# Optimization experiments

Hardware: AMD Instinct MI355X
Metric: run time of the kernel (lower is better)

The kernel has to match this reference:

```python
import jax, jax.numpy as jnp
import numpy as np
from math import sqrt

B, L, S, H, E, D = 2, 2048, 2048, 16, 64, 64

def setup_inputs() -> dict:
    key = jax.random.key(0)
    kq, kk, kv = jax.random.split(key, 3)
    queries = jax.random.normal(kq, (B, L, H, E), dtype=jnp.float32)
    keys = jax.random.normal(kk, (B, S, H, E), dtype=jnp.float32)
    values = jax.random.normal(kv, (B, S, H, D), dtype=jnp.float32)
    # causal mask: True where attention is NOT allowed (j > i), matching masked_fill_ semantics
    causal = jnp.triu(jnp.ones((L, S), dtype=jnp.bool_), k=1)
    attn_mask = jnp.broadcast_to(causal[None, None, :, :], (B, 1, L, S))
    return {"queries": queries, "keys": keys, "values": values, "attn_mask": attn_mask}

def reference(queries, keys, values, attn_mask):
    # scores: [B,H,L,S]
    scale = 1.0 / sqrt(queries.shape[-1])
    scores = jnp.einsum('blhe,bshe->bhls', queries, keys)
    scores = jnp.where(attn_mask, -jnp.inf, scores)
    A = jax.nn.softmax(scale * scores, axis=-1)
    V = jnp.einsum('bhls,bshd->blhd', A, values)
    return V
```

## Files before the change

kernel.cpp:

```cpp
#include <hip/hip_runtime.h>

typedef unsigned short ushort_t;
typedef __attribute__((ext_vector_type(8))) short s8v;
typedef __attribute__((ext_vector_type(2))) unsigned u2v;
typedef __attribute__((ext_vector_type(4))) float f4;

__device__ __forceinline__ ushort_t f2bf(float x) {
    unsigned u = __builtin_bit_cast(unsigned, x);
    return (ushort_t)((u + 0x7FFFu + ((u >> 16) & 1u)) >> 16);
}
__device__ __forceinline__ unsigned pack_hi16(float lo, float hi) {
    unsigned a = __builtin_bit_cast(unsigned, lo);
    unsigned b = __builtin_bit_cast(unsigned, hi);
    return (a >> 16) | (b & 0xFFFF0000u);
}

__global__ __launch_bounds__(256) void prep_kv(const float* __restrict__ K,
                                               const float* __restrict__ V,
                                               ushort_t* __restrict__ Kb,
                                               ushort_t* __restrict__ VT) {
    __shared__ ushort_t T[64 * 72];
    if (blockIdx.x < 2048) {
        const int gid = blockIdx.x * 256 + threadIdx.x;
        const int e = (gid & 7) * 8;
        const int h = (gid >> 3) & 15;
        const int s = (gid >> 7) & 2047;
        const int b = gid >> 18;
        const float* src = K + (((b * 2048 + s) * 16 + h) * 64 + e);
        f4 a = *(const f4*)src;
        f4 c = *(const f4*)(src + 4);
        s8v o;
        #pragma unroll
        for (int j = 0; j < 4; ++j) { o[j] = (short)f2bf(a[j]); o[j + 4] = (short)f2bf(c[j]); }
        *(s8v*)(Kb + (((b * 16 + h) * 2048 + s) * 64 + e)) = o;
    } else {
        const int v = blockIdx.x - 2048;
        const int s0 = (v & 31) * 64;
        const int h  = (v >> 5) & 15;
        const int b  = v >> 9;
        const int t  = threadIdx.x;
        {
            const int srow = t >> 2, dc = (t & 3) * 16;
            const float* src = V + (((b * 2048 + s0 + srow) * 16 + h) * 64 + dc);
            #pragma unroll
            for (int c = 0; c < 4; ++c) {
                f4 vv = *(const f4*)(src + c * 4);
                #pragma unroll
                for (int j = 0; j < 4; ++j) T[(dc + c * 4 + j) * 72 + srow] = f2bf(vv[j]);
            }
        }
        __syncthreads();
        {
            const int d = t >> 2, sq = (t & 3) * 16;
            ushort_t* dst = VT + (((b * 16 + h) * 64 + d) * 2048 + s0 + sq);
            *(s8v*)(dst)     = *(const s8v*)(&T[d * 72 + sq]);
            *(s8v*)(dst + 8) = *(const s8v*)(&T[d * 72 + sq + 8]);
        }
    }
}

__global__ __launch_bounds__(128, 2) void fattn_main(
    const float* __restrict__ Q,
    const ushort_t* __restrict__ Kb,
    const ushort_t* __restrict__ VTb,
    float* __restrict__ O)
{
    constexpr float K1 = 0.18033688011112042f;
    constexpr float SHIFT = 12.0f;
    __shared__ ushort_t KT [64 * 72];
    __shared__ ushort_t VTl[64 * 72];
    __shared__ ushort_t P  [4][16 * 72];

    const int bx = blockIdx.x;
    const int bh = bx & 31;
    const int p  = bx >> 5;
    const int b = bh >> 4, h = bh & 15;

    const int wave = threadIdx.x >> 6;
    const int lane = threadIdx.x & 63;
    const int l15  = lane & 15;
    const int quad = lane >> 4;

    const ushort_t* kb  = Kb  + bh * (2048 * 64);
    const ushort_t* vtb = VTb + bh * (64 * 2048);
    const float*    qb  = Q + b * (2048 * 1024) + h * 64;
    float*          ob  = O + b * (2048 * 1024) + h * 64;

    const s8v ones = {0x3F80, 0x3F80, 0x3F80, 0x3F80, 0x3F80, 0x3F80, 0x3F80, 0x3F80};
    const f4 zero4 = {0.f, 0.f, 0.f, 0.f};

    const int sr = (wave << 5) + (lane >> 1);
    const int sc = (lane & 1) << 5;

    int qr0 = p * 64;

    s8v aq[2][2];
    f4 oacc[2][4];
    f4 lsum[2];

    auto loadQ = [&](int qr) {
        #pragma unroll
        for (int m = 0; m < 2; ++m) {
            const float* qrow = qb + (qr + wave * 32 + m * 16 + l15) * 1024;
            #pragma unroll
            for (int ks = 0; ks < 2; ++ks) {
                f4 x = *(const f4*)(qrow + ks * 32 + quad * 8);
                f4 y = *(const f4*)(qrow + ks * 32 + quad * 8 + 4);
                #pragma unroll
                for (int j = 0; j < 4; ++j) {
                    aq[m][ks][j]     = (short)f2bf(x[j]);
                    aq[m][ks][j + 4] = (short)f2bf(y[j]);
                }
            }
        }
    };
    auto zeroAcc = [&]() {
        #pragma unroll
        for (int m = 0; m < 2; ++m) {
            lsum[m] = zero4;
            #pragma unroll
            for (int d = 0; d < 4; ++d) oacc[m][d] = zero4;
        }
    };
    auto storeO = [&](int qr) {
        #pragma unroll
        for (int m = 0; m < 2; ++m)
            #pragma unroll
            for (int r = 0; r < 4; ++r) {
                const float inv = 1.0f / lsum[m][r];
                const int row = qr + wave * 32 + m * 16 + quad * 4 + r;
                #pragma unroll
                for (int dd = 0; dd < 4; ++dd)
                    ob[row * 1024 + dd * 16 + l15] = oacc[m][dd][r] * inv;
            }
    };

    loadQ(qr0);
    zeroAcc();

    s8v gK[4], gV[4];
    {
        const ushort_t* ksrc = kb + sr * 64 + sc;
        const ushort_t* vsrc = vtb + sr * 2048 + sc;
        #pragma unroll
        for (int c = 0; c < 4; ++c) {
            gK[c] = *(const s8v*)(ksrc + c * 8);
            gV[c] = *(const s8v*)(vsrc + c * 8);
        }
    }

    for (int n = 0; n < 33; ++n) {
        #pragma unroll
        for (int c = 0; c < 4; ++c) {
            *(s8v*)&KT [sr * 72 + sc + c * 8] = gK[c];
            *(s8v*)&VTl[sr * 72 + sc + c * 8] = gV[c];
        }
        __syncthreads();

        s8v gK2[4], gV2[4];
        if (n < 32) {
            const int sn = (n + 1 <= p) ? (n + 1) : (n - p);
            const ushort_t* ksrc = kb + (sn * 64 + sr) * 64 + sc;
            const ushort_t* vsrc = vtb + sr * 2048 + sn * 64 + sc;
            #pragma unroll
            for (int c = 0; c < 4; ++c) {
                gK2[c] = *(const s8v*)(ksrc + c * 8);
                gV2[c] = *(const s8v*)(vsrc + c * 8);
            }
        }

        const int s_cur = (n <= p) ? n : (n - p - 1);
        const int n0 = s_cur * 64;
        const bool diag = (n == p) || (n == 32);

        f4 st[2][4];
        #pragma unroll
        for (int t = 0; t < 4; ++t) {
            const s8v bk0 = *(const s8v*)&KT[(t * 16 + l15) * 72 + quad * 8];
            const s8v bk1 = *(const s8v*)&KT[(t * 16 + l15) * 72 + 32 + quad * 8];
            #pragma unroll
            for (int m = 0; m < 2; ++m) {
                f4 a = __builtin_amdgcn_mfma_f32_16x16x32_bf16(bk0, aq[m][0], zero4, 0, 0, 0);
                st[m][t] = __builtin_amdgcn_mfma_f32_16x16x32_bf16(bk1, aq[m][1], a, 0, 0, 0);
            }
        }

        #pragma unroll
        for (int m = 0; m < 2; ++m) {
            ushort_t* Pm = P[wave * 2 + m];
            #pragma unroll
            for (int t = 0; t < 4; ++t) {
                float pv[4];
                #pragma unroll
                for (int r = 0; r < 4; ++r) {
                    float x = __builtin_fmaf(st[m][t][r], K1, -SHIFT);
                    if (diag) {
                        const int gj = n0 + t * 16 + quad * 4 + r;
                        const int gi = qr0 + wave * 32 + m * 16 + l15;
                        if (gj > gi) x = -INFINITY;
                    }
                    pv[r] = __builtin_exp2f(x);
                }
                u2v pk;
                pk[0] = pack_hi16(pv[0], pv[1]);
                pk[1] = pack_hi16(pv[2], pv[3]);
                *(u2v*)&Pm[l15 * 72 + t * 16 + quad * 4] = pk;
            }
        }

        #pragma unroll
        for (int ks = 0; ks < 2; ++ks) {
            s8v bvv[4];
            #pragma unroll
            for (int dd = 0; dd < 4; ++dd)
                bvv[dd] = *(const s8v*)&VTl[(dd * 16 + l15) * 72 + ks * 32 + quad * 8];
            #pragma unroll
            for (int m = 0; m < 2; ++m) {
                const s8v ap = *(const s8v*)&P[wave * 2 + m][l15 * 72 + ks * 32 + quad * 8];
                lsum[m] = __builtin_amdgcn_mfma_f32_16x16x32_bf16(ap, ones, lsum[m], 0, 0, 0);
                #pragma unroll
                for (int dd = 0; dd < 4; ++dd)
                    oacc[m][dd] = __builtin_amdgcn_mfma_f32_16x16x32_bf16(ap, bvv[dd], oacc[m][dd], 0, 0, 0);
            }
        }

        __syncthreads();

        if (n < 32) {
            #pragma unroll
            for (int c = 0; c < 4; ++c) { gK[c] = gK2[c]; gV[c] = gV2[c]; }
        }

        if (n == p) {
            storeO(qr0);
            qr0 = (31 - p) * 64;
            loadQ(qr0);
            zeroAcc();
        }
    }

    storeO(qr0);
}

#define PSTR 72
__global__ __launch_bounds__(256) void fattn_fallback(
    const float* __restrict__ Q, const float* __restrict__ K,
    const float* __restrict__ V, float* __restrict__ O)
{
    constexpr int strL = 1024, strB = 2048 * strL;
    const float scale = 0.125f;
    __shared__ ushort_t KT[64 * PSTR];
    __shared__ ushort_t VT[64 * PSTR];
    __shared__ ushort_t P[4][16 * PSTR];
    const int bh = blockIdx.x & 31;
    const int b = bh >> 4, h = bh & 15;
    const int im = 31 - (blockIdx.x >> 5);
    const int q0 = im * 64;
    const int tid = threadIdx.x, wave = tid >> 6, lane = tid & 63;
    const int l15 = lane & 15, quad = lane >> 4;
    const float* qbase = Q + b*strB + (q0 + wave*16 + l15)*strL + h*64;
    s8v aq0, aq1;
    {
        f4 q0v = *(const f4*)(qbase + quad*8);
        f4 q1v = *(const f4*)(qbase + quad*8 + 4);
        f4 q2v = *(const f4*)(qbase + 32 + quad*8);
        f4 q3v = *(const f4*)(qbase + 32 + quad*8 + 4);
        #pragma unroll
        for (int j = 0; j < 4; ++j) {
            aq0[j] = (short)f2bf(q0v[j]); aq0[j+4] = (short)f2bf(q1v[j]);
            aq1[j] = (short)f2bf(q2v[j]); aq1[j+4] = (short)f2bf(q3v[j]);
        }
    }
    const f4 zero4 = {0.f,0.f,0.f,0.f};
    f4 oacc[4]; float m_prev[4], lsum[4];
    #pragma unroll
    for (int d = 0; d < 4; ++d) oacc[d] = zero4;
    #pragma unroll
    for (int r = 0; r < 4; ++r) { m_prev[r] = -INFINITY; lsum[r] = 0.0f; }
    const float* kh = K + b*strB + h*64;
    const float* vh = V + b*strB + h*64;
    for (int it = 0; it <= im; ++it) {
        const int n0 = it * 64;
        __syncthreads();
        {
            const float* krow = kh + (n0 + lane)*strL + wave*16;
            f4 k0 = *(const f4*)(krow); f4 k1 = *(const f4*)(krow+4);
            f4 k2 = *(const f4*)(krow+8); f4 k3 = *(const f4*)(krow+12);
            s8v kb0, kb1;
            #pragma unroll
            for (int j = 0; j < 4; ++j) {
                kb0[j] = (short)f2bf(k0[j]); kb0[j+4] = (short)f2bf(k1[j]);
                kb1[j] = (short)f2bf(k2[j]); kb1[j+4] = (short)f2bf(k3[j]);
            }
            *(s8v*)&KT[lane*PSTR + wave*16] = kb0;
            *(s8v*)&KT[lane*PSTR + wave*16 + 8] = kb1;
            const float* vrow = vh + (n0 + lane)*strL + wave*16;
            f4 v0 = *(const f4*)(vrow); f4 v1 = *(const f4*)(vrow+4);
            f4 v2 = *(const f4*)(vrow+8); f4 v3 = *(const f4*)(vrow+12);
            #pragma unroll
            for (int j = 0; j < 4; ++j) {
                VT[(wave*16 + j)*PSTR + lane] = f2bf(v0[j]);
                VT[(wave*16 + 4 + j)*PSTR + lane] = f2bf(v1[j]);
                VT[(wave*16 + 8 + j)*PSTR + lane] = f2bf(v2[j]);
                VT[(wave*16 + 12 + j)*PSTR + lane] = f2bf(v3[j]);
            }
        }
        __syncthreads();
        f4 sacc[4];
        #pragma unroll
        for (int t = 0; t < 4; ++t) {
            sacc[t] = zero4;
            const s8v bk0 = *(const s8v*)&KT[(t*16 + l15)*PSTR + quad*8];
            const s8v bk1 = *(const s8v*)&KT[(t*16 + l15)*PSTR + 32 + quad*8];
            sacc[t] = __builtin_amdgcn_mfma_f32_16x16x32_bf16(aq0, bk0, sacc[t], 0, 0, 0);
            sacc[t] = __builtin_amdgcn_mfma_f32_16x16x32_bf16(aq1, bk1, sacc[t], 0, 0, 0);
        }
        const bool diag = (it == im);
        float sv[4][4], rmax[4];
        #pragma unroll
        for (int r = 0; r < 4; ++r) rmax[r] = -INFINITY;
        #pragma unroll
        for (int t = 0; t < 4; ++t)
            #pragma unroll
            for (int r = 0; r < 4; ++r) {
                float x = sacc[t][r] * scale;
                if (diag) {
                    const int gi = wave*16 + quad*4 + r;
                    const int gj = t*16 + l15;
                    if (gj > gi) x = -INFINITY;
                }
                sv[t][r] = x; rmax[r] = fmaxf(rmax[r], x);
            }
        #pragma unroll
        for (int off = 8; off >= 1; off >>= 1)
            #pragma unroll
            for (int r = 0; r < 4; ++r)
                rmax[r] = fmaxf(rmax[r], __shfl_xor(rmax[r], off, 64));
        float mnew[4], alpha[4], rsum[4];
        #pragma unroll
        for (int r = 0; r < 4; ++r) {
            mnew[r] = fmaxf(m_prev[r], rmax[r]);
            alpha[r] = __expf(m_prev[r] - mnew[r]);
            m_prev[r] = mnew[r]; rsum[r] = 0.f;
        }
        #pragma unroll
        for (int t = 0; t < 4; ++t)
            #pragma unroll
            for (int r = 0; r < 4; ++r) {
                const float p = __expf(sv[t][r] - mnew[r]);
                rsum[r] += p;
                P[wave][(quad*4 + r)*PSTR + t*16 + l15] = f2bf(p);
            }
        #pragma unroll
        for (int off = 8; off >= 1; off >>= 1)
            #pragma unroll
            for (int r = 0; r < 4; ++r)
                rsum[r] += __shfl_xor(rsum[r], off, 64);
        #pragma unroll
        for (int r = 0; r < 4; ++r) lsum[r] = alpha[r]*lsum[r] + rsum[r];
        #pragma unroll
        for (int d = 0; d < 4; ++d)
            #pragma unroll
            for (int r = 0; r < 4; ++r) oacc[d][r] *= alpha[r];
        #pragma unroll
        for (int ks = 0; ks < 2; ++ks) {
            const s8v ap = *(const s8v*)&P[wave][l15*PSTR + ks*32 + quad*8];
            #pragma unroll
            for (int d = 0; d < 4; ++d) {
                const s8v bvv = *(const s8v*)&VT[(d*16 + l15)*PSTR + ks*32 + quad*8];
                oacc[d] = __builtin_amdgcn_mfma_f32_16x16x32_bf16(ap, bvv, oacc[d], 0, 0, 0);
            }
        }
    }
    float* obase = O + b*strB + h*64;
    #pragma unroll
    for (int r = 0; r < 4; ++r) {
        const float inv = 1.0f / lsum[r];
        const int gi = q0 + wave*16 + quad*4 + r;
        #pragma unroll
        for (int d = 0; d < 4; ++d)
            obase[gi*strL + d*16 + l15] = oacc[d][r] * inv;
    }
}

extern "C" void kernel_launch(void* const* d_in, const int* in_sizes, int n_in,
                              void* d_out, int out_size, void* d_ws, size_t ws_size,
                              hipStream_t stream) {
    const float* Q = (const float*)d_in[0];
    const float* K = (const float*)d_in[1];
    const float* V = (const float*)d_in[2];
    float* O = (float*)d_out;
    const size_t NEED = 2ull * 4194304ull * 2ull;
    if (ws_size >= NEED) {
        ushort_t* Kb = (ushort_t*)d_ws;
        ushort_t* VT = Kb + 4194304;
        prep_kv<<<3072, 256, 0, stream>>>(K, V, Kb, VT);
        fattn_main<<<512, 128, 0, stream>>>(Q, Kb, VT, O);
    } else {
        fattn_fallback<<<1024, 256, 0, stream>>>(Q, K, V, O);
    }
}
```

Measured before the change: 176.4 us.

## Grow blocks to 8 waves over 256 query rows with double-buffered K/V tiles

Each block now has 8 waves covering 256 query rows, pairing causal tiles p0 and 7-p0, so every K/V tile staged in LDS is shared by four times as many rows. K/V tiles are double-buffered in LDS, which leaves one barrier per iteration. MFMA sections are wrapped in s_setprio to favor matrix issue. The grid shrinks to 256 blocks, which can under-fill the device's CUs and reduce the number of independent blocks available to hide latency.

Result: slower. 190.9 us (+8.2%).

```diff
diff --git a/kernel.cpp b/kernel.cpp
--- a/kernel.cpp
+++ b/kernel.cpp
@@ -59,7 +59,7 @@
     }
 }
 
-__global__ __launch_bounds__(128, 2) void fattn_main(
+__global__ __launch_bounds__(512, 2) void fattn_main(
     const float* __restrict__ Q,
     const ushort_t* __restrict__ Kb,
     const ushort_t* __restrict__ VTb,
@@ -67,14 +67,15 @@
 {
     constexpr float K1 = 0.18033688011112042f;
     constexpr float SHIFT = 12.0f;
-    __shared__ ushort_t KT [64 * 72];
-    __shared__ ushort_t VTl[64 * 72];
-    __shared__ ushort_t P  [4][16 * 72];
+    __shared__ ushort_t KT[2][64 * 72];
+    __shared__ ushort_t VT[2][64 * 72];
+    __shared__ ushort_t P [8][2][16 * 72];
 
     const int bx = blockIdx.x;
     const int bh = bx & 31;
-    const int p  = bx >> 5;
+    const int p0 = bx >> 5;
     const int b = bh >> 4, h = bh & 15;
+    const int itA = 4 * p0 + 4;
 
     const int wave = threadIdx.x >> 6;
     const int lane = threadIdx.x & 63;
@@ -89,10 +90,10 @@
     const s8v ones = {0x3F80, 0x3F80, 0x3F80, 0x3F80, 0x3F80, 0x3F80, 0x3F80, 0x3F80};
     const f4 zero4 = {0.f, 0.f, 0.f, 0.f};
 
-    const int sr = (wave << 5) + (lane >> 1);
-    const int sc = (lane & 1) << 5;
-
-    int qr0 = p * 64;
+    const int sr = threadIdx.x >> 3;
+    const int sc = (threadIdx.x & 7) * 8;
+
+    int qr0 = p0 * 256;
 
     s8v aq[2][2];
     f4 oacc[2][4];
@@ -138,73 +139,64 @@
     loadQ(qr0);
     zeroAcc();
 
-    s8v gK[4], gV[4];
     {
-        const ushort_t* ksrc = kb + sr * 64 + sc;
-        const ushort_t* vsrc = vtb + sr * 2048 + sc;
-        #pragma unroll
-        for (int c = 0; c < 4; ++c) {
-            gK[c] = *(const s8v*)(ksrc + c * 8);
-            gV[c] = *(const s8v*)(vsrc + c * 8);
-        }
-    }
-
-    for (int n = 0; n < 33; ++n) {
-        #pragma unroll
-        for (int c = 0; c < 4; ++c) {
-            *(s8v*)&KT [sr * 72 + sc + c * 8] = gK[c];
-            *(s8v*)&VTl[sr * 72 + sc + c * 8] = gV[c];
-        }
-        __syncthreads();
-
-        s8v gK2[4], gV2[4];
-        if (n < 32) {
-            const int sn = (n + 1 <= p) ? (n + 1) : (n - p);
-            const ushort_t* ksrc = kb + (sn * 64 + sr) * 64 + sc;
-            const ushort_t* vsrc = vtb + sr * 2048 + sn * 64 + sc;
-            #pragma unroll
-            for (int c = 0; c < 4; ++c) {
-                gK2[c] = *(const s8v*)(ksrc + c * 8);
-                gV2[c] = *(const s8v*)(vsrc + c * 8);
-            }
-        }
-
-        const int s_cur = (n <= p) ? n : (n - p - 1);
-        const int n0 = s_cur * 64;
-        const bool diag = (n == p) || (n == 32);
+        s8v k0 = *(const s8v*)(kb + sr * 64 + sc);
+        s8v v0 = *(const s8v*)(vtb + sr * 2048 + sc);
+        *(s8v*)&KT[0][sr * 72 + sc] = k0;
+        *(s8v*)&VT[0][sr * 72 + sc] = v0;
+    }
+    __syncthreads();
+
+    const ushort_t* ktr = KT[0];  const ushort_t* vtr = VT[0];
+    ushort_t*       ktw = KT[1];  ushort_t*       vtw = VT[1];
+
+    for (int n = 0; n < 36; ++n) {
+        s8v gK2, gV2;
+        if (n < 35) {
+            const int sn1 = (n + 1 < itA) ? (n + 1) : (n + 1 - itA);
+            gK2 = *(const s8v*)(kb + (sn1 * 64 + sr) * 64 + sc);
+            gV2 = *(const s8v*)(vtb + sr * 2048 + sn1 * 64 + sc);
+        }
+
+        const int sn   = (n < itA) ? n : (n - itA);
+        const int tcur = (n < itA) ? p0 : (7 - p0);
+        const bool diag = (sn >= 4 * tcur);
+        const int n0 = sn * 64;
 
         f4 st[2][4];
-        #pragma unroll
-        for (int t = 0; t < 4; ++t) {
-            const s8v bk0 = *(const s8v*)&KT[(t * 16 + l15) * 72 + quad * 8];
-            const s8v bk1 = *(const s8v*)&KT[(t * 16 + l15) * 72 + 32 + quad * 8];
+        __builtin_amdgcn_s_setprio(1);
+        #pragma unroll
+        for (int tq = 0; tq < 4; ++tq) {
+            const s8v bk0 = *(const s8v*)&ktr[(tq * 16 + l15) * 72 + quad * 8];
+            const s8v bk1 = *(const s8v*)&ktr[(tq * 16 + l15) * 72 + 32 + quad * 8];
             #pragma unroll
             for (int m = 0; m < 2; ++m) {
                 f4 a = __builtin_amdgcn_mfma_f32_16x16x32_bf16(bk0, aq[m][0], zero4, 0, 0, 0);
-                st[m][t] = __builtin_amdgcn_mfma_f32_16x16x32_bf16(bk1, aq[m][1], a, 0, 0, 0);
-            }
-        }
+                st[m][tq] = __builtin_amdgcn_mfma_f32_16x16x32_bf16(bk1, aq[m][1], a, 0, 0, 0);
+            }
+        }
+        __builtin_amdgcn_s_setprio(0);
 
         #pragma unroll
         for (int m = 0; m < 2; ++m) {
-            ushort_t* Pm = P[wave * 2 + m];
-            #pragma unroll
-            for (int t = 0; t < 4; ++t) {
-                float pv[4];
+            ushort_t* Pm = P[wave][m];
+            #pragma unroll
+            for (int tq = 0; tq < 4; ++tq) {
+                float pv4[4];
                 #pragma unroll
                 for (int r = 0; r < 4; ++r) {
-                    float x = __builtin_fmaf(st[m][t][r], K1, -SHIFT);
+                    float x = __builtin_fmaf(st[m][tq][r], K1, -SHIFT);
                     if (diag) {
-                        const int gj = n0 + t * 16 + quad * 4 + r;
+                        const int gj = n0 + tq * 16 + quad * 4 + r;
                         const int gi = qr0 + wave * 32 + m * 16 + l15;
                         if (gj > gi) x = -INFINITY;
                     }
-                    pv[r] = __builtin_exp2f(x);
+                    pv4[r] = __builtin_exp2f(x);
                 }
                 u2v pk;
-                pk[0] = pack_hi16(pv[0], pv[1]);
-                pk[1] = pack_hi16(pv[2], pv[3]);
-                *(u2v*)&Pm[l15 * 72 + t * 16 + quad * 4] = pk;
+                pk[0] = pack_hi16(pv4[0], pv4[1]);
+                pk[1] = pack_hi16(pv4[2], pv4[3]);
+                *(u2v*)&Pm[l15 * 72 + tq * 16 + quad * 4] = pk;
             }
         }
 
@@ -213,27 +205,32 @@
             s8v bvv[4];
             #pragma unroll
             for (int dd = 0; dd < 4; ++dd)
-                bvv[dd] = *(const s8v*)&VTl[(dd * 16 + l15) * 72 + ks * 32 + quad * 8];
+                bvv[dd] = *(const s8v*)&vtr[(dd * 16 + l15) * 72 + ks * 32 + quad * 8];
             #pragma unroll
             for (int m = 0; m < 2; ++m) {
-                const s8v ap = *(const s8v*)&P[wave * 2 + m][l15 * 72 + ks * 32 + quad * 8];
+                const s8v ap = *(const s8v*)&P[wave][m][l15 * 72 + ks * 32 + quad * 8];
+                __builtin_amdgcn_s_setprio(1);
                 lsum[m] = __builtin_amdgcn_mfma_f32_16x16x32_bf16(ap, ones, lsum[m], 0, 0, 0);
                 #pragma unroll
                 for (int dd = 0; dd < 4; ++dd)
                     oacc[m][dd] = __builtin_amdgcn_mfma_f32_16x16x32_bf16(ap, bvv[dd], oacc[m][dd], 0, 0, 0);
-            }
+                __builtin_amdgcn_s_setprio(0);
+            }
+        }
+
+        if (n < 35) {
+            *(s8v*)&ktw[sr * 72 + sc] = gK2;
+            *(s8v*)&vtw[sr * 72 + sc] = gV2;
         }
 
         __syncthreads();
 
-        if (n < 32) {
-            #pragma unroll
-            for (int c = 0; c < 4; ++c) { gK[c] = gK2[c]; gV[c] = gV2[c]; }
-        }
-
-        if (n == p) {
+        { ushort_t* t0 = (ushort_t*)ktr; ktr = ktw; ktw = t0; }
+        { ushort_t* t1 = (ushort_t*)vtr; vtr = vtw; vtw = t1; }
+
+        if (n == itA - 1) {
             storeO(qr0);
-            qr0 = (31 - p) * 64;
+            qr0 = (7 - p0) * 256;
             loadQ(qr0);
             zeroAcc();
         }
@@ -395,7 +392,7 @@
         ushort_t* Kb = (ushort_t*)d_ws;
         ushort_t* VT = Kb + 4194304;
         prep_kv<<<3072, 256, 0, stream>>>(K, V, Kb, VT);
-        fattn_main<<<512, 128, 0, stream>>>(Q, Kb, VT, O);
+        fattn_main<<<256, 512, 0, stream>>>(Q, Kb, VT, O);
     } else {
         fattn_fallback<<<1024, 256, 0, stream>>>(Q, K, V, O);
     }
```
